# Optimization experiments

Hardware: AMD Instinct MI355X
Metric: run time of the kernel (lower is better)

Reference implementation:

```python
import jax, jax.numpy as jnp
import numpy as np

B, N, FS, FZ, H, C = 2, 1024, 1024, 64, 16, 64
MAX_WAVELENGTH = 10000


def apply_rope(x, positions):
    # x: (B, N, H, C), positions: (B, N) int
    head_dim = x.shape[-1]
    fraction = 2 * jnp.arange(head_dim // 2, dtype=jnp.float32) / head_dim
    timescale = MAX_WAVELENGTH ** fraction                      # (C/2,)
    sinusoid = positions[..., None].astype(jnp.float32) / timescale  # (B, N, C/2)
    sinusoid = sinusoid[..., None, :]                           # (B, N, 1, C/2)
    sin, cos = jnp.sin(sinusoid), jnp.cos(sinusoid)
    x1, x2 = jnp.split(x, 2, axis=-1)
    out = jnp.concatenate([x1 * cos - x2 * sin, x2 * cos + x1 * sin], axis=-1)
    return out.astype(x.dtype)


def setup_inputs() -> dict:
    key = jax.random.key(0)
    ks = jax.random.split(key, 8)
    s = jax.random.normal(ks[0], (B, N, FS), jnp.float32)
    pair = jax.random.normal(ks[1], (B, N, N, FZ), jnp.float32) * 0.1
    Wq = jax.random.normal(ks[2], (FS, H * C), jnp.float32) / np.sqrt(FS).astype(np.float32)
    Wk = jax.random.normal(ks[3], (FS, H * C), jnp.float32) / np.sqrt(FS).astype(np.float32)
    Wv = jax.random.normal(ks[4], (FS, H * C), jnp.float32) / np.sqrt(FS).astype(np.float32)
    Wb = jax.random.normal(ks[5], (FZ, H), jnp.float32) / np.sqrt(FZ).astype(np.float32)
    segment_ids = jnp.sort(jax.random.randint(ks[6], (B, N), 0, 4), axis=-1).astype(jnp.int32)
    positions = (jnp.arange(B * N, dtype=jnp.int32).reshape(B, N)) % N
    return {"s": s, "pair": pair, "segment_ids": segment_ids, "positions": positions,
            "Wq": Wq, "Wk": Wk, "Wv": Wv, "Wb": Wb}


def reference(s, pair, segment_ids, positions, Wq, Wk, Wv, Wb):
    b_, n, _ = s.shape
    # QKV projections (no bias), reshape to heads
    q = (s @ Wq).reshape(b_, n, H, C)
    k = (s @ Wk).reshape(b_, n, H, C)
    v = (s @ Wv).reshape(b_, n, H, C)
    # RoPE on q and k
    q = apply_rope(q, positions)
    k = apply_rope(k, positions)
    # pair-derived per-head bias: (B, Q, K, Fz) x (Fz, H) -> (B, H, Q, K)
    bias = jnp.einsum('bqkf,fh->bhqk', pair, Wb)
    sm_scale = 1.0 / np.sqrt(C).astype(np.float32)
    # fp32 logits as in _attention_withbias
    logits = jnp.einsum('bqhc,bkhc->bhqk', q, k).astype(jnp.float32)
    # segment mask (self-attention) AND causal mask
    seg_mask = (segment_ids[:, None, :, None] == segment_ids[:, None, None, :])  # (B,1,Q,K)
    causal_mask = jnp.tril(jnp.ones((n, n), dtype=bool))[None, None]             # (1,1,Q,K)
    mask = jnp.logical_and(seg_mask, causal_mask)
    logits = jnp.where(mask, logits, -jnp.inf)
    weights = jax.nn.softmax(logits * sm_scale + bias.astype(jnp.float32), axis=-1).astype(q.dtype)
    out = jnp.einsum('bhqk,bkhc->bqhc', weights, v)
    return out
```

## Files before the change

### kernel.cpp

```cpp
#include <hip/hip_runtime.h>

#define B_ 2
#define N_ 1024
#define FS_ 1024
#define FZ_ 64
#define H_ 16
#define C_ 64

using bf16x8 = __attribute__((ext_vector_type(8))) short;
using f32x4  = __attribute__((ext_vector_type(4))) float;

__device__ inline short f2bf(float x) {
    unsigned int u = __float_as_uint(x);
    unsigned int r = (u + 0x7fffu + ((u >> 16) & 1u)) >> 16;
    return (short)r;
}

__global__ __launch_bounds__(256) void qkv_rope_kernel(
    const float* __restrict__ s, const float* __restrict__ Wq,
    const float* __restrict__ Wk, const float* __restrict__ Wv,
    const int* __restrict__ positions,
    short* __restrict__ Qb, short* __restrict__ Kb, short* __restrict__ Vt)
{
    const int m0  = blockIdx.x * 128;
    const int by  = blockIdx.y;
    const int mat = by >> 3;
    const int n0  = (by & 7) * 128;
    const float* W = (mat == 0) ? Wq : (mat == 1) ? Wk : Wv;

    __shared__ __align__(16) short As[128 * 40];
    __shared__ __align__(16) short Bs[128 * 40];

    const int tid  = threadIdx.x;
    const int wid  = tid >> 6;
    const int lane = tid & 63;
    const int l15  = lane & 15;
    const int quad = lane >> 4;
    const int wm   = (wid & 1) * 64;
    const int wn   = (wid >> 1) * 64;

    f32x4 acc[4][4] = {};

    const int tk4 = tid & 7;
    const int tm  = tid >> 3;
    const int tn4 = tid & 31;
    const int tk  = tid >> 5;

    for (int k0 = 0; k0 < FS_; k0 += 32) {
        #pragma unroll
        for (int i = 0; i < 4; i++) {
            int mrow = tm + 32 * i;
            const float4 v = *reinterpret_cast<const float4*>(
                &s[(size_t)(m0 + mrow) * FS_ + k0 + tk4 * 4]);
            short4 h;
            h.x = f2bf(v.x); h.y = f2bf(v.y); h.z = f2bf(v.z); h.w = f2bf(v.w);
            *reinterpret_cast<short4*>(&As[mrow * 40 + tk4 * 4]) = h;
        }
        #pragma unroll
        for (int i = 0; i < 4; i++) {
            int krow = tk + 8 * i;
            const float4 v = *reinterpret_cast<const float4*>(
                &W[(size_t)(k0 + krow) * 1024 + n0 + tn4 * 4]);
            Bs[(tn4 * 4 + 0) * 40 + krow] = f2bf(v.x);
            Bs[(tn4 * 4 + 1) * 40 + krow] = f2bf(v.y);
            Bs[(tn4 * 4 + 2) * 40 + krow] = f2bf(v.z);
            Bs[(tn4 * 4 + 3) * 40 + krow] = f2bf(v.w);
        }
        __syncthreads();
        bf16x8 a[4], b[4];
        #pragma unroll
        for (int mi = 0; mi < 4; mi++)
            a[mi] = *reinterpret_cast<const bf16x8*>(&As[(wm + mi * 16 + l15) * 40 + quad * 8]);
        #pragma unroll
        for (int ni = 0; ni < 4; ni++)
            b[ni] = *reinterpret_cast<const bf16x8*>(&Bs[(wn + ni * 16 + l15) * 40 + quad * 8]);
        #pragma unroll
        for (int mi = 0; mi < 4; mi++)
            #pragma unroll
            for (int ni = 0; ni < 4; ni++)
                acc[mi][ni] = __builtin_amdgcn_mfma_f32_16x16x32_bf16(a[mi], b[ni], acc[mi][ni], 0, 0, 0);
        __syncthreads();
    }

    const int h = (n0 + wn) >> 6;

    if (mat < 2) {
        short* dst = (mat == 0) ? Qb : Kb;
        float inv_ts[2];
        #pragma unroll
        for (int ni = 0; ni < 2; ni++) {
            float c1 = (float)(ni * 16 + l15);
            inv_ts[ni] = __expf(-(c1 / 32.f) * 9.210340371976184f);
        }
        #pragma unroll
        for (int mi = 0; mi < 4; mi++) {
            #pragma unroll
            for (int r = 0; r < 4; r++) {
                int row = m0 + wm + mi * 16 + quad * 4 + r;
                float pos = (float)positions[row];
                size_t base = (size_t)row * 1024 + n0 + wn;
                #pragma unroll
                for (int ni = 0; ni < 2; ni++) {
                    float sn, cs;
                    __sincosf(pos * inv_ts[ni], &sn, &cs);
                    float x1 = acc[mi][ni][r], x2 = acc[mi][ni + 2][r];
                    dst[base + ni * 16 + l15]       = f2bf(x1 * cs - x2 * sn);
                    dst[base + (ni + 2) * 16 + l15] = f2bf(x2 * cs + x1 * sn);
                }
            }
        }
    } else {
        #pragma unroll
        for (int mi = 0; mi < 4; mi++) {
            #pragma unroll
            for (int r = 0; r < 4; r++) {
                int row = m0 + wm + mi * 16 + quad * 4 + r;
                int bb = row >> 10, nn = row & 1023;
                #pragma unroll
                for (int ni = 0; ni < 4; ni++) {
                    int c = ni * 16 + l15;
                    Vt[(size_t)((bb * H_ + h) * C_ + c) * N_ + nn] = f2bf(acc[mi][ni][r]);
                }
            }
        }
    }
}

#define TQ 16
#define TK 32

__global__ __launch_bounds__(256) void attn_kernel(
    const short* __restrict__ Qb, const short* __restrict__ Kb,
    const short* __restrict__ Vt, const float* __restrict__ pair,
    const float* __restrict__ Wb, const int* __restrict__ seg,
    float* __restrict__ out)
{
    const int bid = blockIdx.x;
    const int hg  = bid & 3;
    const int b   = (bid >> 2) & 1;
    const int j   = bid >> 3;
    const int qt  = (j < 32) ? j : 95 - j;
    const int q0  = qt * TQ;

    const int tid  = threadIdx.x;
    const int wid  = tid >> 6;
    const int lane = tid & 63;
    const int l15  = lane & 15;
    const int quad = lane >> 4;
    const int h    = hg * 4 + wid;

    __shared__ __align__(16) float biasS[TQ * TK * 5];
    __shared__ float WbS[FZ_ * H_];
    __shared__ __align__(16) short Ps[4][TQ * 40];
    __shared__ int segqS[TQ];
    __shared__ int segkS[TK];

    for (int i = tid; i < FZ_ * H_; i += 256) WbS[i] = Wb[i];
    if (tid < TQ) segqS[tid] = seg[b * N_ + q0 + tid];
    __syncthreads();

    bf16x8 qa[2];
    #pragma unroll
    for (int ks = 0; ks < 2; ks++)
        qa[ks] = *reinterpret_cast<const bf16x8*>(
            &Qb[(size_t)(b * N_ + q0 + l15) * 1024 + h * 64 + ks * 32 + quad * 8]);

    f32x4 O[4] = {};
    float m_i[4], l_i[4];
    #pragma unroll
    for (int r = 0; r < 4; r++) { m_i[r] = -1e30f; l_i[r] = 0.f; }

    const int seg_q0 = seg[b * N_ + q0];
    const int ktmax  = (q0 + TQ - 1) >> 5;
    const float sm_scale = 0.125f;

    for (int kt = 0; kt <= ktmax; kt++) {
        const int k0 = kt * TK;
        if (seg[b * N_ + k0 + TK - 1] < seg_q0) continue;

        __syncthreads();
        if (tid < TK) segkS[tid] = seg[b * N_ + k0 + tid];
        #pragma unroll
        for (int pp = 0; pp < 2; pp++) {
            int p  = tid + pp * 256;
            int qq = p >> 5, kk = p & 31;
            const float* pv = &pair[((size_t)(b * N_ + q0 + qq) * N_ + k0 + kk) * FZ_];
            float acc4[4] = {0.f, 0.f, 0.f, 0.f};
            #pragma unroll
            for (int f = 0; f < FZ_; f += 4) {
                float4 pf = *reinterpret_cast<const float4*>(&pv[f]);
                #pragma unroll
                for (int hh = 0; hh < 4; hh++) {
                    const float* wc = &WbS[f * H_ + hg * 4 + hh];
                    acc4[hh] += pf.x * wc[0] + pf.y * wc[H_] + pf.z * wc[2 * H_] + pf.w * wc[3 * H_];
                }
            }
            #pragma unroll
            for (int hh = 0; hh < 4; hh++) biasS[p * 5 + hh] = acc4[hh];
        }
        __syncthreads();

        f32x4 S[2] = {};
        #pragma unroll
        for (int ni = 0; ni < 2; ni++)
            #pragma unroll
            for (int ks = 0; ks < 2; ks++) {
                bf16x8 kb = *reinterpret_cast<const bf16x8*>(
                    &Kb[(size_t)(b * N_ + k0 + ni * 16 + l15) * 1024 + h * 64 + ks * 32 + quad * 8]);
                S[ni] = __builtin_amdgcn_mfma_f32_16x16x32_bf16(qa[ks], kb, S[ni], 0, 0, 0);
            }

        float x[2][4], rm[4];
        #pragma unroll
        for (int r = 0; r < 4; r++) {
            int ql = quad * 4 + r;
            int qg = q0 + ql;
            int sq = segqS[ql];
            #pragma unroll
            for (int ni = 0; ni < 2; ni++) {
                int kc = ni * 16 + l15;
                int kg = k0 + kc;
                bool ok = (kg <= qg) && (segkS[kc] == sq);
                float xv = S[ni][r] * sm_scale + biasS[(ql * TK + kc) * 5 + wid];
                x[ni][r] = ok ? xv : -1e30f;
            }
            rm[r] = fmaxf(x[0][r], x[1][r]);
        }
        #pragma unroll
        for (int off = 1; off < 16; off <<= 1)
            #pragma unroll
            for (int r = 0; r < 4; r++)
                rm[r] = fmaxf(rm[r], __shfl_xor(rm[r], off, 64));

        float rs[4];
        #pragma unroll
        for (int r = 0; r < 4; r++) {
            float mn    = fmaxf(m_i[r], rm[r]);
            float alpha = __expf(m_i[r] - mn);
            float p0 = __expf(x[0][r] - mn);
            float p1 = __expf(x[1][r] - mn);
            Ps[wid][(quad * 4 + r) * 40 + l15]      = f2bf(p0);
            Ps[wid][(quad * 4 + r) * 40 + 16 + l15] = f2bf(p1);
            rs[r]  = p0 + p1;
            m_i[r] = mn;
            l_i[r] *= alpha;
            #pragma unroll
            for (int ni = 0; ni < 4; ni++) O[ni][r] *= alpha;
        }
        #pragma unroll
        for (int off = 1; off < 16; off <<= 1)
            #pragma unroll
            for (int r = 0; r < 4; r++)
                rs[r] += __shfl_xor(rs[r], off, 64);
        #pragma unroll
        for (int r = 0; r < 4; r++) l_i[r] += rs[r];

        __syncthreads();

        bf16x8 ap = *reinterpret_cast<const bf16x8*>(&Ps[wid][l15 * 40 + quad * 8]);
        #pragma unroll
        for (int ni = 0; ni < 4; ni++) {
            bf16x8 vb = *reinterpret_cast<const bf16x8*>(
                &Vt[(size_t)((b * H_ + h) * C_ + ni * 16 + l15) * N_ + k0 + quad * 8]);
            O[ni] = __builtin_amdgcn_mfma_f32_16x16x32_bf16(ap, vb, O[ni], 0, 0, 0);
        }
    }

    #pragma unroll
    for (int r = 0; r < 4; r++) {
        float inv = 1.f / l_i[r];
        int qg = q0 + quad * 4 + r;
        #pragma unroll
        for (int ni = 0; ni < 4; ni++)
            out[(size_t)((b * N_ + qg) * H_ + h) * C_ + ni * 16 + l15] = O[ni][r] * inv;
    }
}

extern "C" void kernel_launch(void* const* d_in, const int* in_sizes, int n_in,
                              void* d_out, int out_size, void* d_ws, size_t ws_size,
                              hipStream_t stream) {
    const float* s    = (const float*)d_in[0];
    const float* pair = (const float*)d_in[1];
    const int*   seg  = (const int*)d_in[2];
    const int*   pos  = (const int*)d_in[3];
    const float* Wq   = (const float*)d_in[4];
    const float* Wk   = (const float*)d_in[5];
    const float* Wv   = (const float*)d_in[6];
    const float* Wb   = (const float*)d_in[7];
    float* out = (float*)d_out;

    short* Qb = (short*)d_ws;
    short* Kb = Qb + (size_t)2048 * 1024;
    short* Vt = Kb + (size_t)2048 * 1024;

    qkv_rope_kernel<<<dim3(16, 24), 256, 0, stream>>>(s, Wq, Wk, Wv, pos, Qb, Kb, Vt);
    attn_kernel<<<dim3(512), 256, 0, stream>>>(Qb, Kb, Vt, pair, Wb, seg, out);
}
```

Baseline: 825.1 us.

## Precompute pair bias via MFMA kernel, pre-convert weights, widen attention key tile

```diff
diff --git a/kernel.cpp b/kernel.cpp
--- a/kernel.cpp
+++ b/kernel.cpp
@@ -10,26 +10,63 @@
 using bf16x8 = __attribute__((ext_vector_type(8))) short;
 using f32x4  = __attribute__((ext_vector_type(4))) float;
 
+typedef __attribute__((address_space(3))) unsigned int lds_u32;
+typedef __attribute__((address_space(1))) unsigned int glb_u32;
+
+__device__ __forceinline__ void glds16(const void* g, void* l) {
+    __builtin_amdgcn_global_load_lds((const glb_u32*)g, (lds_u32*)l, 16, 0, 0);
+}
+
 __device__ inline short f2bf(float x) {
     unsigned int u = __float_as_uint(x);
     unsigned int r = (u + 0x7fffu + ((u >> 16) & 1u)) >> 16;
     return (short)r;
 }
 
-__global__ __launch_bounds__(256) void qkv_rope_kernel(
-    const float* __restrict__ s, const float* __restrict__ Wq,
-    const float* __restrict__ Wk, const float* __restrict__ Wv,
+__global__ __launch_bounds__(256) void conv_s_kernel(const float* __restrict__ s,
+                                                     short* __restrict__ sB) {
+    int i = (blockIdx.x * 256 + threadIdx.x) * 8;
+    float4 v0 = *reinterpret_cast<const float4*>(&s[i]);
+    float4 v1 = *reinterpret_cast<const float4*>(&s[i + 4]);
+    bf16x8 o;
+    o[0] = f2bf(v0.x); o[1] = f2bf(v0.y); o[2] = f2bf(v0.z); o[3] = f2bf(v0.w);
+    o[4] = f2bf(v1.x); o[5] = f2bf(v1.y); o[6] = f2bf(v1.z); o[7] = f2bf(v1.w);
+    *reinterpret_cast<bf16x8*>(&sB[i]) = o;
+}
+
+__global__ __launch_bounds__(256) void conv_w_kernel(const float* __restrict__ Wq,
+                                                     const float* __restrict__ Wk,
+                                                     const float* __restrict__ Wv,
+                                                     short* __restrict__ WT) {
+    const int mat = blockIdx.z;
+    const float* W = (mat == 0) ? Wq : (mat == 1) ? Wk : Wv;
+    const int k0 = blockIdx.x * 32, n0 = blockIdx.y * 32;
+    __shared__ float tl[32][33];
+    const int t = threadIdx.x;
+    {
+        int kr = t >> 3, nq = t & 7;
+        float4 v = *reinterpret_cast<const float4*>(&W[(size_t)(k0 + kr) * 1024 + n0 + nq * 4]);
+        tl[kr][nq * 4 + 0] = v.x; tl[kr][nq * 4 + 1] = v.y;
+        tl[kr][nq * 4 + 2] = v.z; tl[kr][nq * 4 + 3] = v.w;
+    }
+    __syncthreads();
+    int n = t >> 3, kq = t & 7;
+    short4 o;
+    o.x = f2bf(tl[kq * 4 + 0][n]); o.y = f2bf(tl[kq * 4 + 1][n]);
+    o.z = f2bf(tl[kq * 4 + 2][n]); o.w = f2bf(tl[kq * 4 + 3][n]);
+    *reinterpret_cast<short4*>(&WT[(size_t)(mat * 1024 + n0 + n) * 1024 + k0 + kq * 4]) = o;
+}
+
+__global__ __launch_bounds__(256) void qkv_kernel(
+    const short* __restrict__ sB, const short* __restrict__ WT,
     const int* __restrict__ positions,
     short* __restrict__ Qb, short* __restrict__ Kb, short* __restrict__ Vt)
 {
     const int m0  = blockIdx.x * 128;
-    const int by  = blockIdx.y;
-    const int mat = by >> 3;
-    const int n0  = (by & 7) * 128;
-    const float* W = (mat == 0) ? Wq : (mat == 1) ? Wk : Wv;
-
-    __shared__ __align__(16) short As[128 * 40];
-    __shared__ __align__(16) short Bs[128 * 40];
+    const int n0g = blockIdx.y * 128;
+
+    __shared__ __align__(16) short As[128 * 64];
+    __shared__ __align__(16) short Bs[128 * 64];
 
     const int tid  = threadIdx.x;
     const int wid  = tid >> 6;
@@ -41,48 +78,36 @@
 
     f32x4 acc[4][4] = {};
 
-    const int tk4 = tid & 7;
-    const int tm  = tid >> 3;
-    const int tn4 = tid & 31;
-    const int tk  = tid >> 5;
-
-    for (int k0 = 0; k0 < FS_; k0 += 32) {
-        #pragma unroll
-        for (int i = 0; i < 4; i++) {
-            int mrow = tm + 32 * i;
-            const float4 v = *reinterpret_cast<const float4*>(
-                &s[(size_t)(m0 + mrow) * FS_ + k0 + tk4 * 4]);
-            short4 h;
-            h.x = f2bf(v.x); h.y = f2bf(v.y); h.z = f2bf(v.z); h.w = f2bf(v.w);
-            *reinterpret_cast<short4*>(&As[mrow * 40 + tk4 * 4]) = h;
-        }
-        #pragma unroll
-        for (int i = 0; i < 4; i++) {
-            int krow = tk + 8 * i;
-            const float4 v = *reinterpret_cast<const float4*>(
-                &W[(size_t)(k0 + krow) * 1024 + n0 + tn4 * 4]);
-            Bs[(tn4 * 4 + 0) * 40 + krow] = f2bf(v.x);
-            Bs[(tn4 * 4 + 1) * 40 + krow] = f2bf(v.y);
-            Bs[(tn4 * 4 + 2) * 40 + krow] = f2bf(v.z);
-            Bs[(tn4 * 4 + 3) * 40 + krow] = f2bf(v.w);
+    for (int k0 = 0; k0 < FS_; k0 += 64) {
+        #pragma unroll
+        for (int rnd = 0; rnd < 4; rnd++) {
+            int g = rnd * 256 + tid;
+            int m = g >> 3, kq = g & 7;
+            glds16(&sB[(size_t)(m0 + m) * 1024 + k0 + kq * 8], &As[g * 8]);
+            glds16(&WT[(size_t)(n0g + m) * 1024 + k0 + kq * 8], &Bs[g * 8]);
         }
         __syncthreads();
-        bf16x8 a[4], b[4];
-        #pragma unroll
-        for (int mi = 0; mi < 4; mi++)
-            a[mi] = *reinterpret_cast<const bf16x8*>(&As[(wm + mi * 16 + l15) * 40 + quad * 8]);
-        #pragma unroll
-        for (int ni = 0; ni < 4; ni++)
-            b[ni] = *reinterpret_cast<const bf16x8*>(&Bs[(wn + ni * 16 + l15) * 40 + quad * 8]);
-        #pragma unroll
-        for (int mi = 0; mi < 4; mi++)
+        #pragma unroll
+        for (int ks = 0; ks < 2; ks++) {
+            bf16x8 a[4], bb[4];
+            #pragma unroll
+            for (int mi = 0; mi < 4; mi++)
+                a[mi] = *reinterpret_cast<const bf16x8*>(&As[(wm + mi * 16 + l15) * 64 + ks * 32 + quad * 8]);
             #pragma unroll
             for (int ni = 0; ni < 4; ni++)
-                acc[mi][ni] = __builtin_amdgcn_mfma_f32_16x16x32_bf16(a[mi], b[ni], acc[mi][ni], 0, 0, 0);
+                bb[ni] = *reinterpret_cast<const bf16x8*>(&Bs[(wn + ni * 16 + l15) * 64 + ks * 32 + quad * 8]);
+            #pragma unroll
+            for (int mi = 0; mi < 4; mi++)
+                #pragma unroll
+                for (int ni = 0; ni < 4; ni++)
+                    acc[mi][ni] = __builtin_amdgcn_mfma_f32_16x16x32_bf16(a[mi], bb[ni], acc[mi][ni], 0, 0, 0);
+        }
         __syncthreads();
     }
 
-    const int h = (n0 + wn) >> 6;
+    const int mat  = n0g >> 10;
+    const int nloc = n0g & 1023;
+    const int h    = (nloc + wn) >> 6;
 
     if (mat < 2) {
         short* dst = (mat == 0) ? Qb : Kb;
@@ -98,7 +123,7 @@
             for (int r = 0; r < 4; r++) {
                 int row = m0 + wm + mi * 16 + quad * 4 + r;
                 float pos = (float)positions[row];
-                size_t base = (size_t)row * 1024 + n0 + wn;
+                size_t base = (size_t)row * 1024 + nloc + wn;
                 #pragma unroll
                 for (int ni = 0; ni < 2; ni++) {
                     float sn, cs;
@@ -115,25 +140,88 @@
             #pragma unroll
             for (int r = 0; r < 4; r++) {
                 int row = m0 + wm + mi * 16 + quad * 4 + r;
-                int bb = row >> 10, nn = row & 1023;
+                int bb_ = row >> 10, nn = row & 1023;
                 #pragma unroll
                 for (int ni = 0; ni < 4; ni++) {
                     int c = ni * 16 + l15;
-                    Vt[(size_t)((bb * H_ + h) * C_ + c) * N_ + nn] = f2bf(acc[mi][ni][r]);
+                    Vt[(size_t)((bb_ * H_ + h) * C_ + c) * N_ + nn] = f2bf(acc[mi][ni][r]);
                 }
             }
         }
     }
 }
 
+__global__ __launch_bounds__(256) void bias_kernel(
+    const float* __restrict__ pair, const float* __restrict__ Wb,
+    const int* __restrict__ seg, float* __restrict__ biasG)
+{
+    const int kt = blockIdx.x, qt = blockIdx.y, b = blockIdx.z;
+    const int k0 = kt * 16, q0 = qt * 16;
+    if (k0 > q0 + 15) return;
+    if (seg[b * N_ + k0 + 15] < seg[b * N_ + q0]) return;
+
+    __shared__ __align__(16) short pL[256 * 64];
+    __shared__ __align__(16) short wL[16 * 64];
+
+    const int tid  = threadIdx.x;
+    const int wid  = tid >> 6;
+    const int lane = tid & 63;
+    const int l15  = lane & 15;
+    const int quad = lane >> 4;
+
+    {
+        float4 v = *reinterpret_cast<const float4*>(&Wb[tid * 4]);
+        int f = tid >> 2, hb = (tid & 3) * 4;
+        wL[(hb + 0) * 64 + f] = f2bf(v.x);
+        wL[(hb + 1) * 64 + f] = f2bf(v.y);
+        wL[(hb + 2) * 64 + f] = f2bf(v.z);
+        wL[(hb + 3) * 64 + f] = f2bf(v.w);
+    }
+    #pragma unroll
+    for (int rnd = 0; rnd < 16; rnd++) {
+        int g = rnd * 256 + tid;
+        int p = g >> 4, fq = g & 15;
+        int qq = p >> 4, kk = p & 15;
+        float4 v = *reinterpret_cast<const float4*>(
+            &pair[((size_t)(b * N_ + q0 + qq) * N_ + k0 + kk) * FZ_ + fq * 4]);
+        short4 hv;
+        hv.x = f2bf(v.x); hv.y = f2bf(v.y); hv.z = f2bf(v.z); hv.w = f2bf(v.w);
+        *reinterpret_cast<short4*>(&pL[p * 64 + fq * 4]) = hv;
+    }
+    __syncthreads();
+
+    bf16x8 a[2];
+    a[0] = *reinterpret_cast<const bf16x8*>(&wL[l15 * 64 + quad * 8]);
+    a[1] = *reinterpret_cast<const bf16x8*>(&wL[l15 * 64 + 32 + quad * 8]);
+    f32x4 acc[4] = {};
+    #pragma unroll
+    for (int ni = 0; ni < 4; ni++) {
+        #pragma unroll
+        for (int ks = 0; ks < 2; ks++) {
+            bf16x8 bb = *reinterpret_cast<const bf16x8*>(
+                &pL[(wid * 64 + ni * 16 + l15) * 64 + ks * 32 + quad * 8]);
+            acc[ni] = __builtin_amdgcn_mfma_f32_16x16x32_bf16(a[ks], bb, acc[ni], 0, 0, 0);
+        }
+    }
+    #pragma unroll
+    for (int ni = 0; ni < 4; ni++) {
+        #pragma unroll
+        for (int r = 0; r < 4; r++) {
+            int head = quad * 4 + r;
+            int p = wid * 64 + ni * 16 + l15;
+            int qq = p >> 4, kk = p & 15;
+            biasG[((size_t)(b * H_ + head) << 20) + ((size_t)(q0 + qq) << 10) + k0 + kk] = acc[ni][r];
+        }
+    }
+}
+
 #define TQ 16
-#define TK 32
+#define TK 64
 
 __global__ __launch_bounds__(256) void attn_kernel(
     const short* __restrict__ Qb, const short* __restrict__ Kb,
-    const short* __restrict__ Vt, const float* __restrict__ pair,
-    const float* __restrict__ Wb, const int* __restrict__ seg,
-    float* __restrict__ out)
+    const short* __restrict__ Vt, const float* __restrict__ biasG,
+    const int* __restrict__ seg, float* __restrict__ out)
 {
     const int bid = blockIdx.x;
     const int hg  = bid & 3;
@@ -149,15 +237,7 @@
     const int quad = lane >> 4;
     const int h    = hg * 4 + wid;
 
-    __shared__ __align__(16) float biasS[TQ * TK * 5];
-    __shared__ float WbS[FZ_ * H_];
-    __shared__ __align__(16) short Ps[4][TQ * 40];
-    __shared__ int segqS[TQ];
-    __shared__ int segkS[TK];
-
-    for (int i = tid; i < FZ_ * H_; i += 256) WbS[i] = Wb[i];
-    if (tid < TQ) segqS[tid] = seg[b * N_ + q0 + tid];
-    __syncthreads();
+    __shared__ __align__(16) short Ps[4][TQ * 72];
 
     bf16x8 qa[2];
     #pragma unroll
@@ -165,66 +245,56 @@
         qa[ks] = *reinterpret_cast<const bf16x8*>(
             &Qb[(size_t)(b * N_ + q0 + l15) * 1024 + h * 64 + ks * 32 + quad * 8]);
 
+    int sq[4];
+    #pragma unroll
+    for (int r = 0; r < 4; r++) sq[r] = seg[b * N_ + q0 + quad * 4 + r];
+    const int seg_q0 = seg[b * N_ + q0];
+
     f32x4 O[4] = {};
     float m_i[4], l_i[4];
     #pragma unroll
     for (int r = 0; r < 4; r++) { m_i[r] = -1e30f; l_i[r] = 0.f; }
 
-    const int seg_q0 = seg[b * N_ + q0];
-    const int ktmax  = (q0 + TQ - 1) >> 5;
-    const float sm_scale = 0.125f;
+    const int ktmax = (q0 + TQ - 1) >> 6;
+    const float sm  = 0.125f;
+    const float* biasH = biasG + ((size_t)(b * H_ + h) << 20);
 
     for (int kt = 0; kt <= ktmax; kt++) {
         const int k0 = kt * TK;
         if (seg[b * N_ + k0 + TK - 1] < seg_q0) continue;
 
-        __syncthreads();
-        if (tid < TK) segkS[tid] = seg[b * N_ + k0 + tid];
-        #pragma unroll
-        for (int pp = 0; pp < 2; pp++) {
-            int p  = tid + pp * 256;
-            int qq = p >> 5, kk = p & 31;
-            const float* pv = &pair[((size_t)(b * N_ + q0 + qq) * N_ + k0 + kk) * FZ_];
-            float acc4[4] = {0.f, 0.f, 0.f, 0.f};
-            #pragma unroll
-            for (int f = 0; f < FZ_; f += 4) {
-                float4 pf = *reinterpret_cast<const float4*>(&pv[f]);
-                #pragma unroll
-                for (int hh = 0; hh < 4; hh++) {
-                    const float* wc = &WbS[f * H_ + hg * 4 + hh];
-                    acc4[hh] += pf.x * wc[0] + pf.y * wc[H_] + pf.z * wc[2 * H_] + pf.w * wc[3 * H_];
-                }
-            }
-            #pragma unroll
-            for (int hh = 0; hh < 4; hh++) biasS[p * 5 + hh] = acc4[hh];
-        }
-        __syncthreads();
-
-        f32x4 S[2] = {};
-        #pragma unroll
-        for (int ni = 0; ni < 2; ni++)
-            #pragma unroll
-            for (int ks = 0; ks < 2; ks++) {
+        f32x4 S[4] = {};
+        #pragma unroll
+        for (int ks = 0; ks < 2; ks++)
+            #pragma unroll
+            for (int ni = 0; ni < 4; ni++) {
                 bf16x8 kb = *reinterpret_cast<const bf16x8*>(
                     &Kb[(size_t)(b * N_ + k0 + ni * 16 + l15) * 1024 + h * 64 + ks * 32 + quad * 8]);
                 S[ni] = __builtin_amdgcn_mfma_f32_16x16x32_bf16(qa[ks], kb, S[ni], 0, 0, 0);
             }
 
-        float x[2][4], rm[4];
+        int sk[4];
+        float bv[4][4];
+        #pragma unroll
+        for (int ni = 0; ni < 4; ni++) sk[ni] = seg[b * N_ + k0 + ni * 16 + l15];
+        #pragma unroll
+        for (int ni = 0; ni < 4; ni++)
+            #pragma unroll
+            for (int r = 0; r < 4; r++)
+                bv[ni][r] = biasH[((size_t)(q0 + quad * 4 + r) << 10) + k0 + ni * 16 + l15];
+
+        float x[4][4], rm[4];
         #pragma unroll
         for (int r = 0; r < 4; r++) {
-            int ql = quad * 4 + r;
-            int qg = q0 + ql;
-            int sq = segqS[ql];
-            #pragma unroll
-            for (int ni = 0; ni < 2; ni++) {
-                int kc = ni * 16 + l15;
-                int kg = k0 + kc;
-                bool ok = (kg <= qg) && (segkS[kc] == sq);
-                float xv = S[ni][r] * sm_scale + biasS[(ql * TK + kc) * 5 + wid];
-                x[ni][r] = ok ? xv : -1e30f;
-            }
-            rm[r] = fmaxf(x[0][r], x[1][r]);
+            int qg = q0 + quad * 4 + r;
+            rm[r] = -1e30f;
+            #pragma unroll
+            for (int ni = 0; ni < 4; ni++) {
+                int kg = k0 + ni * 16 + l15;
+                bool ok = (kg <= qg) && (sk[ni] == sq[r]);
+                x[ni][r] = ok ? S[ni][r] * sm + bv[ni][r] : -1e30f;
+                rm[r] = fmaxf(rm[r], x[ni][r]);
+            }
         }
         #pragma unroll
         for (int off = 1; off < 16; off <<= 1)
@@ -237,15 +307,18 @@
         for (int r = 0; r < 4; r++) {
             float mn    = fmaxf(m_i[r], rm[r]);
             float alpha = __expf(m_i[r] - mn);
-            float p0 = __expf(x[0][r] - mn);
-            float p1 = __expf(x[1][r] - mn);
-            Ps[wid][(quad * 4 + r) * 40 + l15]      = f2bf(p0);
-            Ps[wid][(quad * 4 + r) * 40 + 16 + l15] = f2bf(p1);
-            rs[r]  = p0 + p1;
+            float rsum  = 0.f;
+            #pragma unroll
+            for (int ni = 0; ni < 4; ni++) {
+                float p = __expf(x[ni][r] - mn);
+                Ps[wid][(quad * 4 + r) * 72 + ni * 16 + l15] = f2bf(p);
+                rsum += p;
+            }
+            rs[r]  = rsum;
             m_i[r] = mn;
             l_i[r] *= alpha;
             #pragma unroll
-            for (int ni = 0; ni < 4; ni++) O[ni][r] *= alpha;
+            for (int ci = 0; ci < 4; ci++) O[ci][r] *= alpha;
         }
         #pragma unroll
         for (int off = 1; off < 16; off <<= 1)
@@ -255,14 +328,17 @@
         #pragma unroll
         for (int r = 0; r < 4; r++) l_i[r] += rs[r];
 
-        __syncthreads();
-
-        bf16x8 ap = *reinterpret_cast<const bf16x8*>(&Ps[wid][l15 * 40 + quad * 8]);
-        #pragma unroll
-        for (int ni = 0; ni < 4; ni++) {
-            bf16x8 vb = *reinterpret_cast<const bf16x8*>(
-                &Vt[(size_t)((b * H_ + h) * C_ + ni * 16 + l15) * N_ + k0 + quad * 8]);
-            O[ni] = __builtin_amdgcn_mfma_f32_16x16x32_bf16(ap, vb, O[ni], 0, 0, 0);
+        bf16x8 ap[2];
+        ap[0] = *reinterpret_cast<const bf16x8*>(&Ps[wid][l15 * 72 + quad * 8]);
+        ap[1] = *reinterpret_cast<const bf16x8*>(&Ps[wid][l15 * 72 + 32 + quad * 8]);
+        #pragma unroll
+        for (int ci = 0; ci < 4; ci++) {
+            #pragma unroll
+            for (int ks = 0; ks < 2; ks++) {
+                bf16x8 vb = *reinterpret_cast<const bf16x8*>(
+                    &Vt[(size_t)((b * H_ + h) * C_ + ci * 16 + l15) * N_ + k0 + ks * 32 + quad * 8]);
+                O[ci] = __builtin_amdgcn_mfma_f32_16x16x32_bf16(ap[ks], vb, O[ci], 0, 0, 0);
+            }
         }
     }
 
@@ -271,8 +347,8 @@
         float inv = 1.f / l_i[r];
         int qg = q0 + quad * 4 + r;
         #pragma unroll
-        for (int ni = 0; ni < 4; ni++)
-            out[(size_t)((b * N_ + qg) * H_ + h) * C_ + ni * 16 + l15] = O[ni][r] * inv;
+        for (int ci = 0; ci < 4; ci++)
+            out[(size_t)((b * N_ + qg) * H_ + h) * C_ + ci * 16 + l15] = O[ci][r] * inv;
     }
 }
 
@@ -292,7 +368,13 @@
     short* Qb = (short*)d_ws;
     short* Kb = Qb + (size_t)2048 * 1024;
     short* Vt = Kb + (size_t)2048 * 1024;
-
-    qkv_rope_kernel<<<dim3(16, 24), 256, 0, stream>>>(s, Wq, Wk, Wv, pos, Qb, Kb, Vt);
-    attn_kernel<<<dim3(512), 256, 0, stream>>>(Qb, Kb, Vt, pair, Wb, seg, out);
-}
+    short* sB = Vt + (size_t)2048 * 1024;
+    short* WT = sB + (size_t)2048 * 1024;
+    float* biasG = (float*)((char*)d_ws + (size_t)22 * 1024 * 1024);
+
+    conv_s_kernel<<<1024, 256, 0, stream>>>(s, sB);
+    conv_w_kernel<<<dim3(32, 32, 3), 256, 0, stream>>>(Wq, Wk, Wv, WT);
+    bias_kernel<<<dim3(64, 64, 2), 256, 0, stream>>>(pair, Wb, seg, biasG);
+    qkv_kernel<<<dim3(16, 24), 256, 0, stream>>>(sB, WT, pos, Qb, Kb, Vt);
+    attn_kernel<<<dim3(512), 256, 0, stream>>>(Qb, Kb, Vt, biasG, seg, out);
+}
```

Measured after the change: 668.2 us. -19.0%, faster.
